# Kernel optimization log

Hardware: AMD Instinct MI355X
Metric: run time of the kernel (lower is better)

Reference implementation:

```python
import jax, jax.numpy as jnp
import numpy as np

IN_FEATURES = 1024
HIDDEN_DIM = 1024
B, S = 4, 4096


def setup_inputs() -> dict:
    key = jax.random.key(0)
    ks = jax.random.split(key, 7)
    lim = 1.0 / np.sqrt(IN_FEATURES)
    x = jax.random.normal(ks[0], (B, S, IN_FEATURES), dtype=jnp.float32)
    Wq = jax.random.uniform(ks[1], (IN_FEATURES, HIDDEN_DIM), jnp.float32, -lim, lim)
    bq = jax.random.uniform(ks[2], (HIDDEN_DIM,), jnp.float32, -lim, lim)
    Wk = jax.random.uniform(ks[3], (IN_FEATURES, HIDDEN_DIM), jnp.float32, -lim, lim)
    bk = jax.random.uniform(ks[4], (HIDDEN_DIM,), jnp.float32, -lim, lim)
    Wv = jax.random.uniform(ks[5], (IN_FEATURES, HIDDEN_DIM), jnp.float32, -lim, lim)
    bv = jax.random.uniform(ks[6], (HIDDEN_DIM,), jnp.float32, -lim, lim)
    return {"x": x, "Wq": Wq, "bq": bq, "Wk": Wk, "bk": bk, "Wv": Wv, "bv": bv}


def reference(x, Wq, bq, Wk, bk, Wv, bv):
    # QKV projections: [B, S, H]
    q = jnp.einsum('bsf,fh->bsh', x, Wq) + bq
    k = jnp.einsum('bsf,fh->bsh', x, Wk) + bk
    v = jnp.einsum('bsf,fh->bsh', x, Wv) + bv
    scale = 1.0 / jnp.sqrt(jnp.asarray(q.shape[-1], dtype=q.dtype))
    scores = jnp.einsum('bqh,bkh->bqk', q, k) * scale  # [B, S, S]
    weights = jax.nn.softmax(scores, axis=-1)
    return jnp.einsum('bqk,bkh->bqh', weights, v)
```

## Files before the change

kernel.cpp:

```cpp
#include <hip/hip_runtime.h>

typedef _Float16 half_t;
typedef _Float16 half4_t __attribute__((ext_vector_type(4)));
typedef _Float16 half8_t __attribute__((ext_vector_type(8)));
typedef float float4_t __attribute__((ext_vector_type(4)));

#define S_LEN 4096
#define NB 4
#define H_DIM 1024

#define MFMA16(a, b, c) __builtin_amdgcn_mfma_f32_16x16x32_f16(a, b, c, 0, 0, 0)

#define BAR_LDS()                                      \
  do {                                                 \
    asm volatile("s_waitcnt lgkmcnt(0)" ::: "memory"); \
    __builtin_amdgcn_s_barrier();                      \
  } while (0)

__global__ __launch_bounds__(256) void wt_prep(
    const float* __restrict__ Wq, const float* __restrict__ Wk,
    const float* __restrict__ Wv, half_t* __restrict__ wth,
    half_t* __restrict__ wtl) {
  const int zi = blockIdx.z;
  const float* W = (zi == 0) ? Wq : (zi == 1) ? Wk : Wv;
  half_t* oh = wth + (size_t)zi * H_DIM * H_DIM;
  half_t* ol = wtl + (size_t)zi * H_DIM * H_DIM;
  const int h0 = blockIdx.x * 32, f0 = blockIdx.y * 32;
  __shared__ float Ws[32][33];
  const int t = threadIdx.x;
  const int c = t & 31, r8 = t >> 5;
#pragma unroll
  for (int rr = 0; rr < 4; rr++)
    Ws[r8 * 4 + rr][c] = W[(size_t)(f0 + r8 * 4 + rr) * H_DIM + h0 + c];
  __syncthreads();
#pragma unroll
  for (int rr = 0; rr < 4; rr++) {
    int h = r8 * 4 + rr;
    float v = Ws[c][h];
    half_t hi = (half_t)v;
    half_t lo = (half_t)(v - (float)hi);
    oh[(size_t)(h0 + h) * H_DIM + f0 + c] = hi;
    ol[(size_t)(h0 + h) * H_DIM + f0 + c] = lo;
  }
}

#define QKV_BK 64

__global__ __launch_bounds__(256, 2) void qkv_mfma(
    const float* __restrict__ x, const half_t* __restrict__ wth,
    const half_t* __restrict__ wtl, const float* __restrict__ bq,
    const float* __restrict__ bk, const float* __restrict__ bv,
    half_t* __restrict__ ws) {
  const int zi = blockIdx.z;
  const half_t* Ah_g = wth + (size_t)zi * H_DIM * H_DIM;
  const half_t* Al_g = wtl + (size_t)zi * H_DIM * H_DIM;
  const float* bias = (zi == 0) ? bq : (zi == 1) ? bk : bv;
  half_t* out = ws + (size_t)zi * ((size_t)NB * S_LEN * H_DIM);
  const int m0 = blockIdx.x * 128;
  const int n0 = blockIdx.y * 128;
  const int t = threadIdx.x;
  const int w = t >> 6, lane = t & 63, ln = lane & 15, quad = lane >> 4;

  __shared__ half_t Bs[16384];

  float4_t acc[2][8] = {};

  const int ss = t >> 1;
  const int fh = (t & 1) * 32;
  const int snt = ss >> 4, sln = ss & 15;

  for (int k0 = 0; k0 < H_DIM; k0 += QKV_BK) {
    half8_t ah[2][2], al[2][2];
#pragma unroll
    for (int i = 0; i < 2; i++) {
      const size_t arow =
          (size_t)(m0 + w * 32 + i * 16 + ln) * H_DIM + k0 + quad * 8;
#pragma unroll
      for (int k2 = 0; k2 < 2; k2++) {
        ah[i][k2] = *(const half8_t*)(Ah_g + arow + k2 * 32);
        al[i][k2] = *(const half8_t*)(Al_g + arow + k2 * 32);
      }
    }
    __syncthreads();
    {
      const float* xp = x + (size_t)(n0 + ss) * H_DIM + k0 + fh;
#pragma unroll
      for (int g = 0; g < 4; g++) {
        float4 v0 = *(const float4*)(xp + g * 8);
        float4 v1 = *(const float4*)(xp + g * 8 + 4);
        float vv[8] = {v0.x, v0.y, v0.z, v0.w, v1.x, v1.y, v1.z, v1.w};
        half8_t hhi, hlo;
#pragma unroll
        for (int j = 0; j < 8; j++) {
          half_t h = (half_t)vv[j];
          hhi[j] = h;
          hlo[j] = (half_t)(vv[j] - (float)h);
        }
        int f = fh + g * 8;
        int k2 = f >> 5, qd = (f >> 3) & 3;
        int base = ((k2 * 8 + snt) * 64 + qd * 16 + sln) * 8;
        *(half8_t*)&Bs[base] = hhi;
        *(half8_t*)&Bs[8192 + base] = hlo;
      }
    }
    __syncthreads();
#pragma unroll
    for (int k2 = 0; k2 < 2; k2++) {
#pragma unroll
      for (int nt = 0; nt < 8; nt++) {
        int base = ((k2 * 8 + nt) * 64 + lane) * 8;
        half8_t bh = *(const half8_t*)&Bs[base];
        half8_t bl = *(const half8_t*)&Bs[8192 + base];
        acc[0][nt] = MFMA16(ah[0][k2], bh, acc[0][nt]);
        acc[1][nt] = MFMA16(ah[1][k2], bh, acc[1][nt]);
        acc[0][nt] = MFMA16(al[0][k2], bh, acc[0][nt]);
        acc[1][nt] = MFMA16(al[1][k2], bh, acc[1][nt]);
        acc[0][nt] = MFMA16(ah[0][k2], bl, acc[0][nt]);
        acc[1][nt] = MFMA16(ah[1][k2], bl, acc[1][nt]);
      }
    }
  }

  const float oscale = (zi == 0) ? 0.03125f : 1.0f;
  float bb[2][4];
#pragma unroll
  for (int i = 0; i < 2; i++)
#pragma unroll
    for (int r = 0; r < 4; r++)
      bb[i][r] = bias[m0 + w * 32 + i * 16 + quad * 4 + r];

  if (zi < 2) {
#pragma unroll
    for (int i = 0; i < 2; i++)
#pragma unroll
      for (int nt = 0; nt < 8; nt++) {
        half4_t h4;
#pragma unroll
        for (int r = 0; r < 4; r++)
          h4[r] = (half_t)((acc[i][nt][r] + bb[i][r]) * oscale);
        size_t s = n0 + nt * 16 + ln;
        *(half4_t*)&out[s * H_DIM + m0 + w * 32 + i * 16 + quad * 4] = h4;
      }
  } else {
#pragma unroll
    for (int i = 0; i < 2; i++)
#pragma unroll
      for (int nt = 0; nt < 8; nt++) {
        int sf = n0 + nt * 16 + ln;
        int b = sf >> 12, si = sf & 4095;
#pragma unroll
        for (int r = 0; r < 4; r++) {
          int h = m0 + w * 32 + i * 16 + quad * 4 + r;
          out[((size_t)b * H_DIM + h) * S_LEN + si] =
              (half_t)(acc[i][nt][r] + bb[i][r]);
        }
      }
  }
}

#define TQ 64
#define TK 128

__global__ __launch_bounds__(512, 2) void flash_attn(
    const half_t* __restrict__ qw, const half_t* __restrict__ kw,
    const half_t* __restrict__ vt, float* __restrict__ out) {
  const int slot = blockIdx.x & 7;
  const int b = slot >> 1;
  const int qb = ((blockIdx.x >> 3) << 1) | (slot & 1);
  const int q0 = qb * TQ;
  const int t = threadIdx.x;
  const int w = t >> 6;
  const int lane = t & 63;
  const int ln = lane & 15;
  const int quad = lane >> 4;

  __shared__ half_t Qs[65536];
  __shared__ half_t Ps[8192];
  __shared__ float wmax[8][64];
  __shared__ float wl[8][64];

  const half_t* qp = qw + ((size_t)b * S_LEN + q0) * H_DIM;
  const half_t* kbp = kw + (size_t)b * S_LEN * H_DIM;
  const half_t* vbt = vt + (size_t)b * H_DIM * S_LEN;

  const half_t* kr = kbp + (size_t)(w * 16 + ln) * H_DIM + quad * 8;
  half8_t kbuf[6];
#pragma unroll
  for (int d = 0; d < 6; d++) kbuf[d] = *(const half8_t*)(kr + d * 32);

#pragma unroll
  for (int i = 0; i < 16; i++) {
    int flat = t * 8 + i * 4096;
    int r = flat >> 10, c = flat & 1023;
    int rs = r >> 4, lq = r & 15, ks = c >> 5, qd = (c >> 3) & 3;
    *(half8_t*)&Qs[((rs * 32 + ks) * 64 + qd * 16 + lq) * 8] =
        *(const half8_t*)&qp[(size_t)r * H_DIM + c];
  }
  BAR_LDS();

  float m_l = -1e30f;
  float l_l = 0.0f;

  float4_t O[4][8] = {};

  for (int kt = 0; kt < S_LEN; kt += TK) {
    float4_t s[4] = {};
    __builtin_amdgcn_s_setprio(1);
#pragma unroll
    for (int ks = 0; ks < 32; ks++) {
      half8_t a0 = *(const half8_t*)&Qs[(ks * 64 + lane) * 8];
      half8_t a1 = *(const half8_t*)&Qs[16384 + (ks * 64 + lane) * 8];
      half8_t a2 = *(const half8_t*)&Qs[32768 + (ks * 64 + lane) * 8];
      half8_t a3 = *(const half8_t*)&Qs[49152 + (ks * 64 + lane) * 8];
      half8_t kc = kbuf[ks % 6];
      if (ks < 26) kbuf[ks % 6] = *(const half8_t*)(kr + (ks + 6) * 32);
      s[0] = MFMA16(a0, kc, s[0]);
      s[1] = MFMA16(a1, kc, s[1]);
      s[2] = MFMA16(a2, kc, s[2]);
      s[3] = MFMA16(a3, kc, s[3]);
    }
    __builtin_amdgcn_s_setprio(0);

    kr += (size_t)TK * H_DIM;
    if (kt + TK < S_LEN) {
#pragma unroll
      for (int d = 0; d < 6; d++) kbuf[d] = *(const half8_t*)(kr + d * 32);
    }

    const half_t* vbase = vbt + (size_t)(w * 128 + ln) * S_LEN + kt + quad * 8;
    half8_t vr[4];
#pragma unroll
    for (int j = 0; j < 4; j++)
      vr[j] = *(const half8_t*)(vbase + (size_t)j * 16 * S_LEN);

    float rm[4][4];
#pragma unroll
    for (int rs = 0; rs < 4; rs++)
#pragma unroll
      for (int r = 0; r < 4; r++) rm[rs][r] = s[rs][r];
#pragma unroll
    for (int off = 1; off < 16; off <<= 1)
#pragma unroll
      for (int rs = 0; rs < 4; rs++)
#pragma unroll
        for (int r = 0; r < 4; r++)
          rm[rs][r] = fmaxf(rm[rs][r], __shfl_xor(rm[rs][r], off));
    if (ln == 0)
#pragma unroll
      for (int rs = 0; rs < 4; rs++)
#pragma unroll
        for (int r = 0; r < 4; r++)
          wmax[w][rs * 16 + quad * 4 + r] = rm[rs][r];
    BAR_LDS();

    float nm_l = m_l;
#pragma unroll
    for (int w2 = 0; w2 < 8; w2++) nm_l = fmaxf(nm_l, wmax[w2][lane]);
    float aS_l = __expf(m_l - nm_l);
    m_l = nm_l;

    const int pbase = (w >> 1) * 512 + (w & 1) * 256 + (ln >> 3) * 128 +
                      quad * 32 + (ln & 7);
    float pl[4][4];
#pragma unroll
    for (int rs = 0; rs < 4; rs++)
#pragma unroll
      for (int r = 0; r < 4; r++) {
        const int q = rs * 16 + quad * 4 + r;
        float nmq = __shfl(m_l, q);
        float aq = __shfl(aS_l, q);
        float p = __expf(s[rs][r] - nmq);
        pl[rs][r] = p;
        Ps[pbase + rs * 2048 + r * 8] = (half_t)p;
#pragma unroll
        for (int j = 0; j < 8; j++) O[rs][j][r] *= aq;
      }
#pragma unroll
    for (int off = 1; off < 16; off <<= 1)
#pragma unroll
      for (int rs = 0; rs < 4; rs++)
#pragma unroll
        for (int r = 0; r < 4; r++) pl[rs][r] += __shfl_xor(pl[rs][r], off);
    if (ln == 0)
#pragma unroll
      for (int rs = 0; rs < 4; rs++)
#pragma unroll
        for (int r = 0; r < 4; r++)
          wl[w][rs * 16 + quad * 4 + r] = pl[rs][r];
    BAR_LDS();

    float s8_l = 0.f;
#pragma unroll
    for (int w2 = 0; w2 < 8; w2++) s8_l += wl[w2][lane];
    l_l = l_l * aS_l + s8_l;

#pragma unroll
    for (int kc = 0; kc < 4; kc++) {
      half8_t pa[4];
#pragma unroll
      for (int rs = 0; rs < 4; rs++)
        pa[rs] = *(const half8_t*)&Ps[((rs * 4 + kc) * 64 + lane) * 8];
      __builtin_amdgcn_s_setprio(1);
#pragma unroll
      for (int j = 0; j < 8; j++) {
        half8_t vc = vr[j & 3];
        const int jn = j + 4;
        if (jn < 8) {
          vr[j & 3] =
              *(const half8_t*)(vbase + (size_t)jn * 16 * S_LEN + kc * 32);
        } else if (kc < 3) {
          vr[j & 3] = *(const half8_t*)(vbase + (size_t)(jn - 8) * 16 * S_LEN +
                                        (kc + 1) * 32);
        }
#pragma unroll
        for (int rs = 0; rs < 4; rs++)
          O[rs][j] = MFMA16(pa[rs], vc, O[rs][j]);
      }
      __builtin_amdgcn_s_setprio(0);
    }
  }

  float il[4][4];
#pragma unroll
  for (int rs = 0; rs < 4; rs++)
#pragma unroll
    for (int r = 0; r < 4; r++)
      il[rs][r] = 1.0f / __shfl(l_l, rs * 16 + quad * 4 + r);
  float* ob = out + ((size_t)b * S_LEN + q0) * H_DIM + w * 128 + ln;
#pragma unroll
  for (int rs = 0; rs < 4; rs++)
#pragma unroll
    for (int j = 0; j < 8; j++)
#pragma unroll
      for (int r = 0; r < 4; r++)
        ob[(size_t)(rs * 16 + quad * 4 + r) * H_DIM + j * 16] =
            O[rs][j][r] * il[rs][r];
}

extern "C" void kernel_launch(void* const* d_in, const int* in_sizes, int n_in,
                              void* d_out, int out_size, void* d_ws,
                              size_t ws_size, hipStream_t stream) {
  const float* x = (const float*)d_in[0];
  const float* Wq = (const float*)d_in[1];
  const float* bq = (const float*)d_in[2];
  const float* Wk = (const float*)d_in[3];
  const float* bk = (const float*)d_in[4];
  const float* Wv = (const float*)d_in[5];
  const float* bv = (const float*)d_in[6];
  half_t* ws = (half_t*)d_ws;
  float* out = (float*)d_out;

  half_t* wth = (half_t*)d_out;
  half_t* wtl = wth + (size_t)3 * H_DIM * H_DIM;

  wt_prep<<<dim3(32, 32, 3), 256, 0, stream>>>(Wq, Wk, Wv, wth, wtl);

  qkv_mfma<<<dim3(8, 128, 3), 256, 0, stream>>>(x, wth, wtl, bq, bk, bv, ws);

  const half_t* qw = ws;
  const half_t* kw = ws + (size_t)NB * S_LEN * H_DIM;
  const half_t* vt = ws + 2 * (size_t)NB * S_LEN * H_DIM;
  flash_attn<<<dim3((S_LEN / TQ) * NB), 512, 0, stream>>>(qw, kw, vt, out);
}
```

Before: 1.075 ms.

## Software-pipeline next tile's QK^T MFMAs with current tile's PV MFMAs

```diff
diff --git a/kernel.cpp b/kernel.cpp
--- a/kernel.cpp
+++ b/kernel.cpp
@@ -202,30 +202,29 @@
   float l_l = 0.0f;
 
   float4_t O[4][8] = {};
+  float4_t s[4] = {};
+
+  __builtin_amdgcn_s_setprio(1);
+#pragma unroll
+  for (int ks = 0; ks < 32; ks++) {
+    half8_t a0 = *(const half8_t*)&Qs[(ks * 64 + lane) * 8];
+    half8_t a1 = *(const half8_t*)&Qs[16384 + (ks * 64 + lane) * 8];
+    half8_t a2 = *(const half8_t*)&Qs[32768 + (ks * 64 + lane) * 8];
+    half8_t a3 = *(const half8_t*)&Qs[49152 + (ks * 64 + lane) * 8];
+    half8_t kc = kbuf[ks % 6];
+    if (ks < 26) kbuf[ks % 6] = *(const half8_t*)(kr + (ks + 6) * 32);
+    s[0] = MFMA16(a0, kc, s[0]);
+    s[1] = MFMA16(a1, kc, s[1]);
+    s[2] = MFMA16(a2, kc, s[2]);
+    s[3] = MFMA16(a3, kc, s[3]);
+  }
+  __builtin_amdgcn_s_setprio(0);
+  kr += (size_t)TK * H_DIM;
+#pragma unroll
+  for (int d = 0; d < 6; d++) kbuf[d] = *(const half8_t*)(kr + d * 32);
 
   for (int kt = 0; kt < S_LEN; kt += TK) {
-    float4_t s[4] = {};
-    __builtin_amdgcn_s_setprio(1);
-#pragma unroll
-    for (int ks = 0; ks < 32; ks++) {
-      half8_t a0 = *(const half8_t*)&Qs[(ks * 64 + lane) * 8];
-      half8_t a1 = *(const half8_t*)&Qs[16384 + (ks * 64 + lane) * 8];
-      half8_t a2 = *(const half8_t*)&Qs[32768 + (ks * 64 + lane) * 8];
-      half8_t a3 = *(const half8_t*)&Qs[49152 + (ks * 64 + lane) * 8];
-      half8_t kc = kbuf[ks % 6];
-      if (ks < 26) kbuf[ks % 6] = *(const half8_t*)(kr + (ks + 6) * 32);
-      s[0] = MFMA16(a0, kc, s[0]);
-      s[1] = MFMA16(a1, kc, s[1]);
-      s[2] = MFMA16(a2, kc, s[2]);
-      s[3] = MFMA16(a3, kc, s[3]);
-    }
-    __builtin_amdgcn_s_setprio(0);
-
-    kr += (size_t)TK * H_DIM;
-    if (kt + TK < S_LEN) {
-#pragma unroll
-      for (int d = 0; d < 6; d++) kbuf[d] = *(const half8_t*)(kr + d * 32);
-    }
+    const bool notlast = (kt + TK < S_LEN);
 
     const half_t* vbase = vbt + (size_t)(w * 128 + ln) * S_LEN + kt + quad * 8;
     half8_t vr[4];
@@ -294,23 +293,68 @@
     for (int w2 = 0; w2 < 8; w2++) s8_l += wl[w2][lane];
     l_l = l_l * aS_l + s8_l;
 
-#pragma unroll
-    for (int kc = 0; kc < 4; kc++) {
+    if (notlast) {
+      s[0] = (float4_t){0.f, 0.f, 0.f, 0.f};
+      s[1] = s[0];
+      s[2] = s[0];
+      s[3] = s[0];
       half8_t pa[4];
-#pragma unroll
-      for (int rs = 0; rs < 4; rs++)
-        pa[rs] = *(const half8_t*)&Ps[((rs * 4 + kc) * 64 + lane) * 8];
       __builtin_amdgcn_s_setprio(1);
 #pragma unroll
-      for (int j = 0; j < 8; j++) {
+      for (int u = 0; u < 32; u++) {
+        const int kc2 = u >> 3, j = u & 7;
+        if ((u & 7) == 0) {
+#pragma unroll
+          for (int rs = 0; rs < 4; rs++)
+            pa[rs] = *(const half8_t*)&Ps[((rs * 4 + kc2) * 64 + lane) * 8];
+        }
         half8_t vc = vr[j & 3];
         const int jn = j + 4;
         if (jn < 8) {
           vr[j & 3] =
-              *(const half8_t*)(vbase + (size_t)jn * 16 * S_LEN + kc * 32);
-        } else if (kc < 3) {
+              *(const half8_t*)(vbase + (size_t)jn * 16 * S_LEN + kc2 * 32);
+        } else if (kc2 < 3) {
           vr[j & 3] = *(const half8_t*)(vbase + (size_t)(jn - 8) * 16 * S_LEN +
-                                        (kc + 1) * 32);
+                                        (kc2 + 1) * 32);
+        }
+        half8_t a0 = *(const half8_t*)&Qs[(u * 64 + lane) * 8];
+        half8_t a1 = *(const half8_t*)&Qs[16384 + (u * 64 + lane) * 8];
+        half8_t a2 = *(const half8_t*)&Qs[32768 + (u * 64 + lane) * 8];
+        half8_t a3 = *(const half8_t*)&Qs[49152 + (u * 64 + lane) * 8];
+        half8_t kk = kbuf[u % 6];
+        if (u < 26) kbuf[u % 6] = *(const half8_t*)(kr + (u + 6) * 32);
+        s[0] = MFMA16(a0, kk, s[0]);
+        O[0][j] = MFMA16(pa[0], vc, O[0][j]);
+        s[1] = MFMA16(a1, kk, s[1]);
+        O[1][j] = MFMA16(pa[1], vc, O[1][j]);
+        s[2] = MFMA16(a2, kk, s[2]);
+        O[2][j] = MFMA16(pa[2], vc, O[2][j]);
+        s[3] = MFMA16(a3, kk, s[3]);
+        O[3][j] = MFMA16(pa[3], vc, O[3][j]);
+      }
+      __builtin_amdgcn_s_setprio(0);
+      kr += (size_t)TK * H_DIM;
+#pragma unroll
+      for (int d = 0; d < 6; d++) kbuf[d] = *(const half8_t*)(kr + d * 32);
+    } else {
+      half8_t pa[4];
+      __builtin_amdgcn_s_setprio(1);
+#pragma unroll
+      for (int u = 0; u < 32; u++) {
+        const int kc2 = u >> 3, j = u & 7;
+        if ((u & 7) == 0) {
+#pragma unroll
+          for (int rs = 0; rs < 4; rs++)
+            pa[rs] = *(const half8_t*)&Ps[((rs * 4 + kc2) * 64 + lane) * 8];
+        }
+        half8_t vc = vr[j & 3];
+        const int jn = j + 4;
+        if (jn < 8) {
+          vr[j & 3] =
+              *(const half8_t*)(vbase + (size_t)jn * 16 * S_LEN + kc2 * 32);
+        } else if (kc2 < 3) {
+          vr[j & 3] = *(const half8_t*)(vbase + (size_t)(jn - 8) * 16 * S_LEN +
+                                        (kc2 + 1) * 32);
         }
 #pragma unroll
         for (int rs = 0; rs < 4; rs++)
```

Measured after the change: 1.880 ms. 1.75x slower.
